# Kernel tuning notes

Hardware: AMD Instinct MI355X
Metric: run time of the kernel (lower is better)

Reference implementation:

```python
import jax, jax.numpy as jnp
import numpy as np

B = 64           # images
C = 100          # num_categories
LOOP = 3         # LOOP_NUM: max boxes per (image, category)
NB_PER = 150     # boxes per image
N = B * NB_PER   # total boxes
FEAT = 2052      # 2048 backbone feats + 4 bbox coords
OUT = 2048       # gcn_output_shape


def _occ_slots(key):
    """For each element, its occurrence index among equal-valued keys (stable order)."""
    n = key.shape[0]
    order = jnp.argsort(key, stable=True)
    sk = key[order]
    idx = jnp.arange(n)
    is_new = jnp.concatenate([jnp.ones((1,), bool), sk[1:] != sk[:-1]])
    run_start = jax.lax.cummax(jnp.where(is_new, idx, 0))
    pos = idx - run_start
    return jnp.zeros(n, dtype=jnp.int32).at[order].set(pos.astype(jnp.int32))


def setup_inputs() -> dict:
    key = jax.random.key(0)
    ks = jax.random.split(key, 8)
    image_features = jax.random.normal(ks[0], (N, 2048), jnp.float32)
    bbox_list = jax.random.uniform(ks[1], (N, 4), jnp.float32)
    global_features = jax.random.normal(ks[2], (B, C), jnp.float32)
    adj = jax.random.uniform(ks[3], (B, C, C), jnp.float32)
    X = jnp.full((C, C), 1e-6, jnp.float32)                 # nn.Parameter init
    lin_w = jax.random.normal(ks[4], (LOOP,), jnp.float32) * 0.5   # Linear(3,1) weight
    lin_b = jax.random.normal(ks[5], (), jnp.float32) * 0.1        # Linear(3,1) bias
    gc_w = jax.random.normal(ks[6], (FEAT, OUT), jnp.float32) / np.sqrt(FEAT)
    gc_b = jnp.zeros((OUT,), jnp.float32)
    # labels cycle 1..C so each (image, category) appears <= ceil(NB_PER/C)=2 <= LOOP times
    label_list = (jnp.arange(N, dtype=jnp.int32) % C) + 1
    batch = (jnp.arange(N, dtype=jnp.int32) // NB_PER)
    return dict(image_features=image_features, bbox_list=bbox_list,
                global_features=global_features, adj=adj, X=X,
                lin_w=lin_w, lin_b=lin_b, gc_w=gc_w, gc_b=gc_b,
                label_list=label_list, batch=batch)


def reference(image_features, bbox_list, global_features, adj, X,
              lin_w, lin_b, gc_w, gc_b, label_list, batch):
    # full_features = concat(backbone feats, bbox): [N, 2052]
    full = jnp.concatenate([image_features, bbox_list], axis=1)
    cat = label_list - 1
    # occurrence slot of each box within its (image, category) bucket
    slots = _occ_slots(batch.astype(jnp.int64) * C + cat.astype(jnp.int64))
    # scatter-build gcn_input: [B, C, LOOP, 2052]
    gcn_input = jnp.zeros((B, C, LOOP, FEAT), full.dtype).at[batch, cat, slots].set(full)
    # transpose(2,3) then Linear(LOOP -> 1) and squeeze: [B, C, 2052]
    x = jnp.einsum('bcld,l->bcd', gcn_input, lin_w) + lin_b
    # new_adj = X + adj; GraphConvolution: adj @ (x @ W) + b, then leaky_relu
    new_adj = X[None, :, :] + adj
    support = jnp.einsum('bcd,do->bco', x, gc_w)          # [B, C, 2048]
    gcn_out = jax.nn.leaky_relu(jnp.einsum('bcn,bno->bco', new_adj, support) + gc_b)
    # attention aggregate: [B,1,C] @ [B,C,OUT] -> [B,OUT]
    return jnp.einsum('bc,bco->bo', global_features, gcn_out)
```

## Files before the change

kernel.cpp:

```cpp
#include <hip/hip_runtime.h>
#include <stdint.h>

#define BB    64
#define CC    100
#define NBPER 150
#define FEAT  2052
#define KP    2112
#define NOUT  2048
#define MR    6400

typedef __attribute__((ext_vector_type(8))) short   short8;
typedef __attribute__((ext_vector_type(4))) float   floatx4;

__device__ __forceinline__ unsigned short f2bf(float f) {
  unsigned int u = __float_as_uint(f);
  u += 0x7FFFu + ((u >> 16) & 1u);
  return (unsigned short)(u >> 16);
}

__device__ __forceinline__ void async16(const void* g, void* l) {
  __builtin_amdgcn_global_load_lds((__attribute__((address_space(1))) void*)(g),
                                   (__attribute__((address_space(3))) void*)(l),
                                   16, 0, 0);
}

__global__ __launch_bounds__(256) void k_transpose(const float* __restrict__ gcw,
                                                   unsigned short* __restrict__ gcwT) {
  __shared__ float tile[32][33];
  const int ko = blockIdx.x;
  const int oo = blockIdx.y;
  const int tx = threadIdx.x, ty = threadIdx.y;
#pragma unroll
  for (int i = 0; i < 4; ++i) {
    const int k = ko * 32 + ty + i * 8;
    const int o = oo * 32 + tx;
    tile[ty + i * 8][tx] = (k < FEAT) ? gcw[(size_t)k * NOUT + o] : 0.f;
  }
  __syncthreads();
#pragma unroll
  for (int i = 0; i < 4; ++i) {
    const int o = oo * 32 + ty + i * 8;
    const int k = ko * 32 + tx;
    gcwT[(size_t)o * KP + k] = f2bf(tile[tx][ty + i * 8]);
  }
}

__global__ __launch_bounds__(256) void k_buildx(const float* __restrict__ imgf,
                                                const float* __restrict__ bbox,
                                                const float* __restrict__ lw,
                                                const float* __restrict__ lb,
                                                const int* __restrict__ labels,
                                                unsigned short* __restrict__ xbf) {
  __shared__ int lab[NBPER];
  __shared__ int sidx[3];
  const int c = blockIdx.x, b = blockIdx.y;
  const int tid = threadIdx.x;
  if (tid < NBPER) lab[tid] = labels[b * NBPER + tid];
  __syncthreads();
  if (tid == 0) {
    int cnt = 0; sidx[0] = -1; sidx[1] = -1; sidx[2] = -1;
    for (int i = 0; i < NBPER; ++i)
      if (lab[i] == c + 1 && cnt < 3) { sidx[cnt] = b * NBPER + i; ++cnt; }
  }
  __syncthreads();
  const int r = b * CC + c;
  const int i0 = sidx[0], i1 = sidx[1], i2 = sidx[2];
  const float w0 = lw[0], w1 = lw[1], w2 = lw[2], bias = lb[0];
  for (int s = tid; s < KP / 8; s += 256) {
    const int d0 = s * 8;
    float v[8];
#pragma unroll
    for (int q = 0; q < 8; ++q) v[q] = 0.f;
    if (d0 < 2048) {
      if (i0 >= 0) {
        const float4* p = (const float4*)(imgf + (size_t)i0 * 2048 + d0);
        float4 u0 = p[0], u1 = p[1];
        v[0] += w0 * u0.x; v[1] += w0 * u0.y; v[2] += w0 * u0.z; v[3] += w0 * u0.w;
        v[4] += w0 * u1.x; v[5] += w0 * u1.y; v[6] += w0 * u1.z; v[7] += w0 * u1.w;
      }
      if (i1 >= 0) {
        const float4* p = (const float4*)(imgf + (size_t)i1 * 2048 + d0);
        float4 u0 = p[0], u1 = p[1];
        v[0] += w1 * u0.x; v[1] += w1 * u0.y; v[2] += w1 * u0.z; v[3] += w1 * u0.w;
        v[4] += w1 * u1.x; v[5] += w1 * u1.y; v[6] += w1 * u1.z; v[7] += w1 * u1.w;
      }
      if (i2 >= 0) {
        const float4* p = (const float4*)(imgf + (size_t)i2 * 2048 + d0);
        float4 u0 = p[0], u1 = p[1];
        v[0] += w2 * u0.x; v[1] += w2 * u0.y; v[2] += w2 * u0.z; v[3] += w2 * u0.w;
        v[4] += w2 * u1.x; v[5] += w2 * u1.y; v[6] += w2 * u1.z; v[7] += w2 * u1.w;
      }
#pragma unroll
      for (int q = 0; q < 8; ++q) v[q] += bias;
    } else if (d0 == 2048) {
      if (i0 >= 0) { float4 u = *(const float4*)(bbox + (size_t)i0 * 4);
        v[0] += w0 * u.x; v[1] += w0 * u.y; v[2] += w0 * u.z; v[3] += w0 * u.w; }
      if (i1 >= 0) { float4 u = *(const float4*)(bbox + (size_t)i1 * 4);
        v[0] += w1 * u.x; v[1] += w1 * u.y; v[2] += w1 * u.z; v[3] += w1 * u.w; }
      if (i2 >= 0) { float4 u = *(const float4*)(bbox + (size_t)i2 * 4);
        v[0] += w2 * u.x; v[1] += w2 * u.y; v[2] += w2 * u.z; v[3] += w2 * u.w; }
      v[0] += bias; v[1] += bias; v[2] += bias; v[3] += bias;
    }
    unsigned short o[8] __attribute__((aligned(16)));
#pragma unroll
    for (int q = 0; q < 8; ++q) o[q] = f2bf(v[q]);
    *(uint4*)(xbf + (size_t)r * KP + d0) = *(const uint4*)o;
  }
}

__global__ __launch_bounds__(256) void k_gemm1(const unsigned short* __restrict__ A,
                                               const unsigned short* __restrict__ Bt,
                                               unsigned short* __restrict__ ST) {
  __shared__ unsigned short shbuf[128 * 132] __attribute__((aligned(16)));
  unsigned short* Asm = shbuf;
  unsigned short* Bsm = shbuf + 8192;
  const int tid  = threadIdx.x;
  const int lane = tid & 63;
  const int w    = tid >> 6;
  const int v    = blockIdx.y * gridDim.x + blockIdx.x;
  const int ncol = (v & 7) * 2 + ((v >> 3) & 1);
  const int mrow = v >> 4;
  const int m0   = mrow * 128;
  const int n0   = ncol * 128;
  const int wm   = (w & 1) * 64;
  const int wn   = (w >> 1) * 64;
  const int srow = lane >> 3;
  const int gk   = (((lane & 7) - srow) & 7) * 8;
  const int quad = lane >> 4;
  const int lrow = lane & 15;
  const int rot  = (lane & 7) * 8;

  floatx4 acc[4][4] = {};

  for (int kb = 0; kb < KP / 64; ++kb) {
    const int k0 = kb * 64;
#pragma unroll
    for (int t = 0; t < 4; ++t) {
      const int chunk = t * 4 + w;
      const int row = chunk * 8 + srow;
      async16(A  + (size_t)(m0 + row) * KP + (k0 + gk), &Asm[chunk * 512]);
      async16(Bt + (size_t)(n0 + row) * KP + (k0 + gk), &Bsm[chunk * 512]);
    }
    __syncthreads();
#pragma unroll
    for (int kp = 0; kp < 2; ++kp) {
      const int koff = (kp * 32 + quad * 8 + rot) & 63;
      short8 af[4], bfr[4];
#pragma unroll
      for (int i = 0; i < 4; ++i)
        af[i]  = *(const short8*)&Asm[(wm + i * 16 + lrow) * 64 + koff];
#pragma unroll
      for (int j = 0; j < 4; ++j)
        bfr[j] = *(const short8*)&Bsm[(wn + j * 16 + lrow) * 64 + koff];
#pragma unroll
      for (int i = 0; i < 4; ++i)
#pragma unroll
        for (int j = 0; j < 4; ++j)
          acc[i][j] = __builtin_amdgcn_mfma_f32_16x16x32_bf16(af[i], bfr[j], acc[i][j], 0, 0, 0);
    }
    __syncthreads();
  }

#pragma unroll
  for (int j = 0; j < 4; ++j) {
    const int ol = wn + j * 16 + lrow;
#pragma unroll
    for (int i = 0; i < 4; ++i) {
#pragma unroll
      for (int rr = 0; rr < 4; ++rr) {
        const int ml = wm + i * 16 + quad * 4 + rr;
        shbuf[ol * 132 + ml] = f2bf(acc[i][j][rr]);
      }
    }
  }
  __syncthreads();
#pragma unroll
  for (int it = 0; it < 32; ++it) {
    const int idx = it * 256 + tid;
    const int o = idx >> 6;
    const int cp = idx & 63;
    const int m = 2 * cp;
    const int r = m0 + m;
    const int b = r / 100;
    const int c = r - b * 100;
    const unsigned int val = *(const unsigned int*)&shbuf[o * 132 + m];
    *(unsigned int*)&ST[((size_t)b * NOUT + n0 + o) * 128 + c] = val;
  }
}

__global__ __launch_bounds__(256) void k_gemm2(const float* __restrict__ X,
                                               const float* __restrict__ adj,
                                               const unsigned short* __restrict__ ST,
                                               const float* __restrict__ gf,
                                               const float* __restrict__ gcb,
                                               float* __restrict__ outp) {
  __shared__ unsigned short A2s[128 * 64] __attribute__((aligned(16)));
  __shared__ unsigned short Ssm[128 * 64] __attribute__((aligned(16)));
  __shared__ float gsm[128];
  __shared__ float red[128 * 9];
  const int tid = threadIdx.x;
  const int o0  = blockIdx.x * 128;
  const int b   = blockIdx.y;
  if (tid < 128) gsm[tid] = (tid < CC) ? gf[b * CC + tid] : 0.f;

  const int lane = tid & 63;
  const int w    = tid >> 6;
  const int srow = lane >> 3;
  const int gk   = (((lane & 7) - srow) & 7) * 8;
  const int quad = lane >> 4;
  const int lrow = lane & 15;
  const int rot  = (lane & 7) * 8;
  const int wm   = (w & 1) * 64;
  const int wn   = (w >> 1) * 64;

  floatx4 acc[4][4] = {};

  for (int kb = 0; kb < 2; ++kb) {
    const int k0 = kb * 64;
    __syncthreads();
#pragma unroll
    for (int t = 0; t < 4; ++t) {
      const int chunk = t * 4 + w;
      const int orow = chunk * 8 + srow;
      async16(ST + ((size_t)b * NOUT + o0 + orow) * 128 + k0 + gk, &Ssm[chunk * 512]);
    }
    {
      const int ngrp = tid & 15;
      const int cb   = tid >> 4;
      const int n    = k0 + ngrp * 4;
#pragma unroll
      for (int it = 0; it < 8; ++it) {
        const int c = it * 16 + cb;
        unsigned short pk[4] __attribute__((aligned(8))) = {0, 0, 0, 0};
        if (c < CC && n < CC) {
          const float4 a4 = *(const float4*)(adj + (size_t)b * (CC * CC) + c * CC + n);
          const float4 x4 = *(const float4*)(X + c * CC + n);
          pk[0] = f2bf(a4.x + x4.x); pk[1] = f2bf(a4.y + x4.y);
          pk[2] = f2bf(a4.z + x4.z); pk[3] = f2bf(a4.w + x4.w);
        }
        *(uint2*)&A2s[c * 64 + ((ngrp * 4 + 8 * (c & 7)) & 63)] = *(const uint2*)pk;
      }
    }
    __syncthreads();
#pragma unroll
    for (int kp = 0; kp < 2; ++kp) {
      const int koff = (kp * 32 + quad * 8 + rot) & 63;
      short8 af[4], bfr[4];
#pragma unroll
      for (int i = 0; i < 4; ++i)
        af[i]  = *(const short8*)&A2s[(wm + i * 16 + lrow) * 64 + koff];
#pragma unroll
      for (int j = 0; j < 4; ++j)
        bfr[j] = *(const short8*)&Ssm[(wn + j * 16 + lrow) * 64 + koff];
#pragma unroll
      for (int i = 0; i < 4; ++i)
#pragma unroll
        for (int j = 0; j < 4; ++j)
          acc[i][j] = __builtin_amdgcn_mfma_f32_16x16x32_bf16(af[i], bfr[j], acc[i][j], 0, 0, 0);
    }
  }
  __syncthreads();

  const int slot = (w & 1) * 4 + quad;
#pragma unroll
  for (int j = 0; j < 4; ++j) {
    const int ol = wn + j * 16 + lrow;
    const float bias = gcb[o0 + ol];
    float s = 0.f;
#pragma unroll
    for (int i = 0; i < 4; ++i) {
#pragma unroll
      for (int rr = 0; rr < 4; ++rr) {
        const int c = wm + i * 16 + quad * 4 + rr;
        float t = acc[i][j][rr] + bias;
        t = (t > 0.f) ? t : 0.01f * t;
        s += gsm[c] * t;
      }
    }
    red[ol * 9 + slot] = s;
  }
  __syncthreads();
  if (tid < 128) {
    float s = 0.f;
#pragma unroll
    for (int t = 0; t < 8; ++t) s += red[tid * 9 + t];
    outp[(size_t)b * NOUT + o0 + tid] = s;
  }
}

extern "C" void kernel_launch(void* const* d_in, const int* in_sizes, int n_in,
                              void* d_out, int out_size, void* d_ws, size_t ws_size,
                              hipStream_t stream) {
  const float* imgf   = (const float*)d_in[0];
  const float* bbox   = (const float*)d_in[1];
  const float* gfeat  = (const float*)d_in[2];
  const float* adj    = (const float*)d_in[3];
  const float* X      = (const float*)d_in[4];
  const float* lw     = (const float*)d_in[5];
  const float* lb     = (const float*)d_in[6];
  const float* gcw    = (const float*)d_in[7];
  const float* gcb    = (const float*)d_in[8];
  const int*   labels = (const int*)d_in[9];

  char* ws = (char*)d_ws;
  unsigned short* xbf      = (unsigned short*)(ws);
  unsigned short* gcwT     = (unsigned short*)(ws + 27033600);
  unsigned short* supportT = (unsigned short*)(ws + 35684352);
  float*          outp     = (float*)d_out;

  k_transpose<<<dim3(KP / 32, NOUT / 32), dim3(32, 8), 0, stream>>>(gcw, gcwT);
  k_buildx<<<dim3(CC, BB), dim3(256), 0, stream>>>(imgf, bbox, lw, lb, labels, xbf);
  k_gemm1<<<dim3(16, 50), dim3(256), 0, stream>>>(xbf, gcwT, supportT);
  k_gemm2<<<dim3(NOUT / 128, BB), dim3(256), 0, stream>>>(X, adj, supportT, gfeat, gcb, outp);
}
```

Measured before the change: 294.0 us.

## Merge prep kernels and prefetch next K tile into registers in GEMM1

```diff
diff --git a/kernel.cpp b/kernel.cpp
--- a/kernel.cpp
+++ b/kernel.cpp
@@ -24,37 +24,43 @@
                                    16, 0, 0);
 }
 
-__global__ __launch_bounds__(256) void k_transpose(const float* __restrict__ gcw,
-                                                   unsigned short* __restrict__ gcwT) {
+__global__ __launch_bounds__(256) void k_prep(const float* __restrict__ gcw,
+                                              unsigned short* __restrict__ gcwT,
+                                              const float* __restrict__ imgf,
+                                              const float* __restrict__ bbox,
+                                              const float* __restrict__ lw,
+                                              const float* __restrict__ lb,
+                                              const int* __restrict__ labels,
+                                              unsigned short* __restrict__ xbf) {
   __shared__ float tile[32][33];
-  const int ko = blockIdx.x;
-  const int oo = blockIdx.y;
-  const int tx = threadIdx.x, ty = threadIdx.y;
-#pragma unroll
-  for (int i = 0; i < 4; ++i) {
-    const int k = ko * 32 + ty + i * 8;
-    const int o = oo * 32 + tx;
-    tile[ty + i * 8][tx] = (k < FEAT) ? gcw[(size_t)k * NOUT + o] : 0.f;
-  }
-  __syncthreads();
-#pragma unroll
-  for (int i = 0; i < 4; ++i) {
-    const int o = oo * 32 + ty + i * 8;
-    const int k = ko * 32 + tx;
-    gcwT[(size_t)o * KP + k] = f2bf(tile[tx][ty + i * 8]);
-  }
-}
-
-__global__ __launch_bounds__(256) void k_buildx(const float* __restrict__ imgf,
-                                                const float* __restrict__ bbox,
-                                                const float* __restrict__ lw,
-                                                const float* __restrict__ lb,
-                                                const int* __restrict__ labels,
-                                                unsigned short* __restrict__ xbf) {
   __shared__ int lab[NBPER];
   __shared__ int sidx[3];
-  const int c = blockIdx.x, b = blockIdx.y;
+  const int bx = blockIdx.x;
   const int tid = threadIdx.x;
+
+  if (bx < 4224) {
+    const int ko = bx % 66;
+    const int oo = bx / 66;
+    const int tx = tid & 31, ty = tid >> 5;
+#pragma unroll
+    for (int i = 0; i < 4; ++i) {
+      const int k = ko * 32 + ty + i * 8;
+      const int o = oo * 32 + tx;
+      tile[ty + i * 8][tx] = (k < FEAT) ? gcw[(size_t)k * NOUT + o] : 0.f;
+    }
+    __syncthreads();
+#pragma unroll
+    for (int i = 0; i < 4; ++i) {
+      const int o = oo * 32 + ty + i * 8;
+      const int k = ko * 32 + tx;
+      gcwT[(size_t)o * KP + k] = f2bf(tile[tx][ty + i * 8]);
+    }
+    return;
+  }
+
+  const int r2 = bx - 4224;
+  const int b = r2 / 100;
+  const int c = r2 - b * 100;
   if (tid < NBPER) lab[tid] = labels[b * NBPER + tid];
   __syncthreads();
   if (tid == 0) {
@@ -108,9 +114,9 @@
   }
 }
 
-__global__ __launch_bounds__(256) void k_gemm1(const unsigned short* __restrict__ A,
-                                               const unsigned short* __restrict__ Bt,
-                                               unsigned short* __restrict__ ST) {
+__global__ __launch_bounds__(256, 1) void k_gemm1(const unsigned short* __restrict__ A,
+                                                  const unsigned short* __restrict__ Bt,
+                                                  unsigned short* __restrict__ ST) {
   __shared__ unsigned short shbuf[128 * 132] __attribute__((aligned(16)));
   unsigned short* Asm = shbuf;
   unsigned short* Bsm = shbuf + 8192;
@@ -130,18 +136,38 @@
   const int lrow = lane & 15;
   const int rot  = (lane & 7) * 8;
 
+  size_t aoff[4], boff[4];
+  int ldsoff[4];
+#pragma unroll
+  for (int t = 0; t < 4; ++t) {
+    const int chunk = t * 4 + w;
+    const int row = chunk * 8 + srow;
+    aoff[t] = (size_t)(m0 + row) * KP + gk;
+    boff[t] = (size_t)(n0 + row) * KP + gk;
+    ldsoff[t] = chunk * 512 + lane * 8;
+  }
+
   floatx4 acc[4][4] = {};
 
+#pragma unroll
+  for (int t = 0; t < 4; ++t) {
+    const int chunk = t * 4 + w;
+    async16(A  + aoff[t], &Asm[chunk * 512]);
+    async16(Bt + boff[t], &Bsm[chunk * 512]);
+  }
+  __syncthreads();
+
   for (int kb = 0; kb < KP / 64; ++kb) {
-    const int k0 = kb * 64;
-#pragma unroll
-    for (int t = 0; t < 4; ++t) {
-      const int chunk = t * 4 + w;
-      const int row = chunk * 8 + srow;
-      async16(A  + (size_t)(m0 + row) * KP + (k0 + gk), &Asm[chunk * 512]);
-      async16(Bt + (size_t)(n0 + row) * KP + (k0 + gk), &Bsm[chunk * 512]);
-    }
-    __syncthreads();
+    const bool more = (kb + 1) < (KP / 64);
+    uint4 pa[4], pb[4];
+    if (more) {
+      const int knext = (kb + 1) * 64;
+#pragma unroll
+      for (int t = 0; t < 4; ++t) {
+        pa[t] = *(const uint4*)(A  + aoff[t] + knext);
+        pb[t] = *(const uint4*)(Bt + boff[t] + knext);
+      }
+    }
 #pragma unroll
     for (int kp = 0; kp < 2; ++kp) {
       const int koff = (kp * 32 + quad * 8 + rot) & 63;
@@ -159,6 +185,14 @@
           acc[i][j] = __builtin_amdgcn_mfma_f32_16x16x32_bf16(af[i], bfr[j], acc[i][j], 0, 0, 0);
     }
     __syncthreads();
+    if (more) {
+#pragma unroll
+      for (int t = 0; t < 4; ++t) {
+        *(uint4*)&Asm[ldsoff[t]] = pa[t];
+        *(uint4*)&Bsm[ldsoff[t]] = pb[t];
+      }
+      __syncthreads();
+    }
   }
 
 #pragma unroll
@@ -308,8 +342,7 @@
   unsigned short* supportT = (unsigned short*)(ws + 35684352);
   float*          outp     = (float*)d_out;
 
-  k_transpose<<<dim3(KP / 32, NOUT / 32), dim3(32, 8), 0, stream>>>(gcw, gcwT);
-  k_buildx<<<dim3(CC, BB), dim3(256), 0, stream>>>(imgf, bbox, lw, lb, labels, xbf);
+  k_prep<<<dim3(4224 + 6400), dim3(256), 0, stream>>>(gcw, gcwT, imgf, bbox, lw, lb, labels, xbf);
   k_gemm1<<<dim3(16, 50), dim3(256), 0, stream>>>(xbf, gcwT, supportT);
   k_gemm2<<<dim3(NOUT / 128, BB), dim3(256), 0, stream>>>(X, adj, supportT, gfeat, gcb, outp);
 }
```

Result: slower. 487.9 us (+66.0%).

## Merge prep kernels and precompute bf16 adjacency for async loading in gemm2

Applied to the files above, without the earlier changes.

```diff
diff --git a/kernel.cpp b/kernel.cpp
--- a/kernel.cpp
+++ b/kernel.cpp
@@ -24,87 +24,128 @@
                                    16, 0, 0);
 }
 
-__global__ __launch_bounds__(256) void k_transpose(const float* __restrict__ gcw,
-                                                   unsigned short* __restrict__ gcwT) {
+__global__ __launch_bounds__(256) void k_prep(const float* __restrict__ gcw,
+                                              unsigned short* __restrict__ gcwT,
+                                              const float* __restrict__ imgf,
+                                              const float* __restrict__ bbox,
+                                              const float* __restrict__ lw,
+                                              const float* __restrict__ lb,
+                                              const int* __restrict__ labels,
+                                              unsigned short* __restrict__ xbf,
+                                              const float* __restrict__ X,
+                                              const float* __restrict__ adj,
+                                              unsigned short* __restrict__ A2p) {
   __shared__ float tile[32][33];
-  const int ko = blockIdx.x;
-  const int oo = blockIdx.y;
-  const int tx = threadIdx.x, ty = threadIdx.y;
-#pragma unroll
-  for (int i = 0; i < 4; ++i) {
-    const int k = ko * 32 + ty + i * 8;
-    const int o = oo * 32 + tx;
-    tile[ty + i * 8][tx] = (k < FEAT) ? gcw[(size_t)k * NOUT + o] : 0.f;
-  }
-  __syncthreads();
-#pragma unroll
-  for (int i = 0; i < 4; ++i) {
-    const int o = oo * 32 + ty + i * 8;
-    const int k = ko * 32 + tx;
-    gcwT[(size_t)o * KP + k] = f2bf(tile[tx][ty + i * 8]);
-  }
-}
-
-__global__ __launch_bounds__(256) void k_buildx(const float* __restrict__ imgf,
-                                                const float* __restrict__ bbox,
-                                                const float* __restrict__ lw,
-                                                const float* __restrict__ lb,
-                                                const int* __restrict__ labels,
-                                                unsigned short* __restrict__ xbf) {
   __shared__ int lab[NBPER];
-  __shared__ int sidx[3];
-  const int c = blockIdx.x, b = blockIdx.y;
+  __shared__ int sidx2[25][3];
+  const int bx  = blockIdx.x;
   const int tid = threadIdx.x;
-  if (tid < NBPER) lab[tid] = labels[b * NBPER + tid];
-  __syncthreads();
-  if (tid == 0) {
-    int cnt = 0; sidx[0] = -1; sidx[1] = -1; sidx[2] = -1;
-    for (int i = 0; i < NBPER; ++i)
-      if (lab[i] == c + 1 && cnt < 3) { sidx[cnt] = b * NBPER + i; ++cnt; }
-  }
-  __syncthreads();
-  const int r = b * CC + c;
-  const int i0 = sidx[0], i1 = sidx[1], i2 = sidx[2];
-  const float w0 = lw[0], w1 = lw[1], w2 = lw[2], bias = lb[0];
-  for (int s = tid; s < KP / 8; s += 256) {
-    const int d0 = s * 8;
-    float v[8];
-#pragma unroll
-    for (int q = 0; q < 8; ++q) v[q] = 0.f;
-    if (d0 < 2048) {
-      if (i0 >= 0) {
-        const float4* p = (const float4*)(imgf + (size_t)i0 * 2048 + d0);
-        float4 u0 = p[0], u1 = p[1];
-        v[0] += w0 * u0.x; v[1] += w0 * u0.y; v[2] += w0 * u0.z; v[3] += w0 * u0.w;
-        v[4] += w0 * u1.x; v[5] += w0 * u1.y; v[6] += w0 * u1.z; v[7] += w0 * u1.w;
-      }
-      if (i1 >= 0) {
-        const float4* p = (const float4*)(imgf + (size_t)i1 * 2048 + d0);
-        float4 u0 = p[0], u1 = p[1];
-        v[0] += w1 * u0.x; v[1] += w1 * u0.y; v[2] += w1 * u0.z; v[3] += w1 * u0.w;
-        v[4] += w1 * u1.x; v[5] += w1 * u1.y; v[6] += w1 * u1.z; v[7] += w1 * u1.w;
-      }
-      if (i2 >= 0) {
-        const float4* p = (const float4*)(imgf + (size_t)i2 * 2048 + d0);
-        float4 u0 = p[0], u1 = p[1];
-        v[0] += w2 * u0.x; v[1] += w2 * u0.y; v[2] += w2 * u0.z; v[3] += w2 * u0.w;
-        v[4] += w2 * u1.x; v[5] += w2 * u1.y; v[6] += w2 * u1.z; v[7] += w2 * u1.w;
-      }
-#pragma unroll
-      for (int q = 0; q < 8; ++q) v[q] += bias;
-    } else if (d0 == 2048) {
-      if (i0 >= 0) { float4 u = *(const float4*)(bbox + (size_t)i0 * 4);
-        v[0] += w0 * u.x; v[1] += w0 * u.y; v[2] += w0 * u.z; v[3] += w0 * u.w; }
-      if (i1 >= 0) { float4 u = *(const float4*)(bbox + (size_t)i1 * 4);
-        v[0] += w1 * u.x; v[1] += w1 * u.y; v[2] += w1 * u.z; v[3] += w1 * u.w; }
-      if (i2 >= 0) { float4 u = *(const float4*)(bbox + (size_t)i2 * 4);
-        v[0] += w2 * u.x; v[1] += w2 * u.y; v[2] += w2 * u.z; v[3] += w2 * u.w; }
-      v[0] += bias; v[1] += bias; v[2] += bias; v[3] += bias;
-    }
-    unsigned short o[8] __attribute__((aligned(16)));
-#pragma unroll
-    for (int q = 0; q < 8; ++q) o[q] = f2bf(v[q]);
-    *(uint4*)(xbf + (size_t)r * KP + d0) = *(const uint4*)o;
+
+  if (bx < 4224) {
+    const int ko = bx % 66;
+    const int oo = bx / 66;
+    const int tx = tid & 31, ty = tid >> 5;
+#pragma unroll
+    for (int i = 0; i < 4; ++i) {
+      const int k = ko * 32 + ty + i * 8;
+      const int o = oo * 32 + tx;
+      tile[ty + i * 8][tx] = (k < FEAT) ? gcw[(size_t)k * NOUT + o] : 0.f;
+    }
+    __syncthreads();
+#pragma unroll
+    for (int i = 0; i < 4; ++i) {
+      const int o = oo * 32 + ty + i * 8;
+      const int k = ko * 32 + tx;
+      gcwT[(size_t)o * KP + k] = f2bf(tile[tx][ty + i * 8]);
+    }
+    return;
+  }
+
+  if (bx < 4480) {
+    const int r2 = bx - 4224;
+    const int b  = r2 >> 2;
+    const int cg = r2 & 3;
+    if (tid < NBPER) lab[tid] = labels[b * NBPER + tid];
+    __syncthreads();
+    if (tid < 25) {
+      const int c = cg * 25 + tid;
+      int cnt = 0, o0 = -1, o1 = -1, o2 = -1;
+      for (int i = 0; i < NBPER; ++i) {
+        if (lab[i] == c + 1) {
+          if (cnt == 0) o0 = b * NBPER + i;
+          else if (cnt == 1) o1 = b * NBPER + i;
+          else if (cnt == 2) o2 = b * NBPER + i;
+          ++cnt;
+        }
+      }
+      sidx2[tid][0] = o0; sidx2[tid][1] = o1; sidx2[tid][2] = o2;
+    }
+    __syncthreads();
+    const float w0 = lw[0], w1 = lw[1], w2 = lw[2], bias = lb[0];
+    for (int cl = 0; cl < 25; ++cl) {
+      const int c = cg * 25 + cl;
+      const int r = b * CC + c;
+      const int i0 = sidx2[cl][0], i1 = sidx2[cl][1], i2 = sidx2[cl][2];
+      for (int s = tid; s < KP / 8; s += 256) {
+        const int d0 = s * 8;
+        float v[8];
+#pragma unroll
+        for (int q = 0; q < 8; ++q) v[q] = 0.f;
+        if (d0 < 2048) {
+          if (i0 >= 0) {
+            const float4* p = (const float4*)(imgf + (size_t)i0 * 2048 + d0);
+            float4 u0 = p[0], u1 = p[1];
+            v[0] += w0 * u0.x; v[1] += w0 * u0.y; v[2] += w0 * u0.z; v[3] += w0 * u0.w;
+            v[4] += w0 * u1.x; v[5] += w0 * u1.y; v[6] += w0 * u1.z; v[7] += w0 * u1.w;
+          }
+          if (i1 >= 0) {
+            const float4* p = (const float4*)(imgf + (size_t)i1 * 2048 + d0);
+            float4 u0 = p[0], u1 = p[1];
+            v[0] += w1 * u0.x; v[1] += w1 * u0.y; v[2] += w1 * u0.z; v[3] += w1 * u0.w;
+            v[4] += w1 * u1.x; v[5] += w1 * u1.y; v[6] += w1 * u1.z; v[7] += w1 * u1.w;
+          }
+          if (i2 >= 0) {
+            const float4* p = (const float4*)(imgf + (size_t)i2 * 2048 + d0);
+            float4 u0 = p[0], u1 = p[1];
+            v[0] += w2 * u0.x; v[1] += w2 * u0.y; v[2] += w2 * u0.z; v[3] += w2 * u0.w;
+            v[4] += w2 * u1.x; v[5] += w2 * u1.y; v[6] += w2 * u1.z; v[7] += w2 * u1.w;
+          }
+#pragma unroll
+          for (int q = 0; q < 8; ++q) v[q] += bias;
+        } else if (d0 == 2048) {
+          if (i0 >= 0) { float4 u = *(const float4*)(bbox + (size_t)i0 * 4);
+            v[0] += w0 * u.x; v[1] += w0 * u.y; v[2] += w0 * u.z; v[3] += w0 * u.w; }
+          if (i1 >= 0) { float4 u = *(const float4*)(bbox + (size_t)i1 * 4);
+            v[0] += w1 * u.x; v[1] += w1 * u.y; v[2] += w1 * u.z; v[3] += w1 * u.w; }
+          if (i2 >= 0) { float4 u = *(const float4*)(bbox + (size_t)i2 * 4);
+            v[0] += w2 * u.x; v[1] += w2 * u.y; v[2] += w2 * u.z; v[3] += w2 * u.w; }
+          v[0] += bias; v[1] += bias; v[2] += bias; v[3] += bias;
+        }
+        unsigned short o[8] __attribute__((aligned(16)));
+#pragma unroll
+        for (int q = 0; q < 8; ++q) o[q] = f2bf(v[q]);
+        *(uint4*)(xbf + (size_t)r * KP + d0) = *(const uint4*)o;
+      }
+    }
+    return;
+  }
+
+  {
+    const int b = bx - 4480;
+#pragma unroll
+    for (int it = 0; it < 16; ++it) {
+      const int idx = it * 256 + tid;
+      const int c = idx >> 5, ng = idx & 31;
+      const int n = ng * 4;
+      unsigned short pk[4] __attribute__((aligned(8))) = {0, 0, 0, 0};
+      if (c < CC && n < CC) {
+        const float4 a4 = *(const float4*)(adj + (size_t)b * (CC * CC) + c * CC + n);
+        const float4 x4 = *(const float4*)(X + c * CC + n);
+        pk[0] = f2bf(a4.x + x4.x); pk[1] = f2bf(a4.y + x4.y);
+        pk[2] = f2bf(a4.z + x4.z); pk[3] = f2bf(a4.w + x4.w);
+      }
+      *(uint2*)&A2p[((size_t)b * 128 + c) * 128 + n] = *(const uint2*)pk;
+    }
   }
 }
 
@@ -188,8 +229,7 @@
   }
 }
 
-__global__ __launch_bounds__(256) void k_gemm2(const float* __restrict__ X,
-                                               const float* __restrict__ adj,
+__global__ __launch_bounds__(256) void k_gemm2(const unsigned short* __restrict__ A2p,
                                                const unsigned short* __restrict__ ST,
                                                const float* __restrict__ gf,
                                                const float* __restrict__ gcb,
@@ -221,25 +261,9 @@
 #pragma unroll
     for (int t = 0; t < 4; ++t) {
       const int chunk = t * 4 + w;
-      const int orow = chunk * 8 + srow;
-      async16(ST + ((size_t)b * NOUT + o0 + orow) * 128 + k0 + gk, &Ssm[chunk * 512]);
-    }
-    {
-      const int ngrp = tid & 15;
-      const int cb   = tid >> 4;
-      const int n    = k0 + ngrp * 4;
-#pragma unroll
-      for (int it = 0; it < 8; ++it) {
-        const int c = it * 16 + cb;
-        unsigned short pk[4] __attribute__((aligned(8))) = {0, 0, 0, 0};
-        if (c < CC && n < CC) {
-          const float4 a4 = *(const float4*)(adj + (size_t)b * (CC * CC) + c * CC + n);
-          const float4 x4 = *(const float4*)(X + c * CC + n);
-          pk[0] = f2bf(a4.x + x4.x); pk[1] = f2bf(a4.y + x4.y);
-          pk[2] = f2bf(a4.z + x4.z); pk[3] = f2bf(a4.w + x4.w);
-        }
-        *(uint2*)&A2s[c * 64 + ((ngrp * 4 + 8 * (c & 7)) & 63)] = *(const uint2*)pk;
-      }
+      const int row = chunk * 8 + srow;
+      async16(A2p + ((size_t)b * 128 + row) * 128 + k0 + gk, &A2s[chunk * 512]);
+      async16(ST + ((size_t)b * NOUT + o0 + row) * 128 + k0 + gk, &Ssm[chunk * 512]);
     }
     __syncthreads();
 #pragma unroll
@@ -306,10 +330,11 @@
   unsigned short* xbf      = (unsigned short*)(ws);
   unsigned short* gcwT     = (unsigned short*)(ws + 27033600);
   unsigned short* supportT = (unsigned short*)(ws + 35684352);
+  unsigned short* A2p      = (unsigned short*)(ws + 69238784);
   float*          outp     = (float*)d_out;
 
-  k_transpose<<<dim3(KP / 32, NOUT / 32), dim3(32, 8), 0, stream>>>(gcw, gcwT);
-  k_buildx<<<dim3(CC, BB), dim3(256), 0, stream>>>(imgf, bbox, lw, lb, labels, xbf);
+  k_prep<<<dim3(4544), dim3(256), 0, stream>>>(gcw, gcwT, imgf, bbox, lw, lb,
+                                               labels, xbf, X, adj, A2p);
   k_gemm1<<<dim3(16, 50), dim3(256), 0, stream>>>(xbf, gcwT, supportT);
-  k_gemm2<<<dim3(NOUT / 128, BB), dim3(256), 0, stream>>>(X, adj, supportT, gfeat, gcb, outp);
-}
+  k_gemm2<<<dim3(NOUT / 128, BB), dim3(256), 0, stream>>>(A2p, supportT, gfeat, gcb, outp);
+}
```

New measurement: 298.1 us. About the same (+1.4%).
